# Performance work log

Measured on AMD Instinct MI355X. Metric: run time of the kernel, lower is better.

Reference implementation:

```python
import jax, jax.numpy as jnp
import numpy as np

B, L, D, H = 2, 2048, 2048, 16
HD = D // H  # 128

def setup_inputs() -> dict:
    key = jax.random.key(0)
    ks = jax.random.split(key, 12)
    s = 1.0 / np.sqrt(D)
    inp = {
        'x': jax.random.normal(ks[0], (B, L, D), jnp.float32),
        'sin': jax.random.normal(ks[1], (L, HD // 2), jnp.float32),
        'cos': jax.random.normal(ks[2], (L, HD // 2), jnp.float32),
        'mask': jnp.tril(jnp.ones((L, L), jnp.int32))[None, None],  # causal [1,1,L,L]
        'Wq': jax.random.normal(ks[3], (D, D), jnp.float32) * s,
        'bq': jnp.zeros((D,), jnp.float32),
        'Wk': jax.random.normal(ks[4], (D, D), jnp.float32) * s,
        'bk': jnp.zeros((D,), jnp.float32),
        'Wv': jax.random.normal(ks[5], (D, D), jnp.float32) * s,
        'bv': jnp.zeros((D,), jnp.float32),
        'Wo': jax.random.normal(ks[6], (D, D), jnp.float32) * s,
        'bo': jnp.zeros((D,), jnp.float32),
    }
    return inp

def reference(x, sin, cos, mask, Wq, bq, Wk, bk, Wv, bv, Wo, bo):
    Bx, Lx, Dx = x.shape
    q = (x @ Wq.T + bq).reshape(Bx, Lx, H, HD)
    k = (x @ Wk.T + bk).reshape(Bx, Lx, H, HD)
    v = (x @ Wv.T + bv).reshape(Bx, Lx, H, HD)
    half = HD // 2
    # partial rotary: note original computes q_rot*(cos - sin) (faithful)
    rot = (cos - sin)[:, None, :]  # [L,1,half]
    q = jnp.concatenate([q[..., :half] * rot, q[..., half:]], axis=-1)
    k = jnp.concatenate([k[..., :half] * rot, k[..., half:]], axis=-1)
    q = q.transpose(0, 2, 1, 3)  # [B,H,L,hd]
    k = k.transpose(0, 2, 1, 3)
    v = v.transpose(0, 2, 1, 3)
    scores = jnp.einsum('bhqd,bhkd->bhqk', q, k) / np.sqrt(HD).astype(np.float32)
    scores = jnp.where(mask == 0, -jnp.inf, scores)
    attn = jax.nn.softmax(scores, axis=-1)
    out = jnp.einsum('bhqk,bhkd->bhqd', attn, v)
    out = out.transpose(0, 2, 1, 3).reshape(Bx, Lx, Dx)
    return out @ Wo.T + bo
```

## Files before the change

kernel.cpp:

```cpp
#include <hip/hip_runtime.h>
#include <hip/hip_bf16.h>

typedef __attribute__((ext_vector_type(8))) short short8;
typedef __attribute__((ext_vector_type(4))) ushort ushort4v;
typedef __attribute__((ext_vector_type(4))) float f32x4;

#define MFMA16(A, B, C) __builtin_amdgcn_mfma_f32_16x16x32_bf16(A, B, C, 0, 0, 0)

#define GLOAD16(gp, lp)                                        \
  __builtin_amdgcn_global_load_lds(                            \
      (__attribute__((address_space(1))) void*)(gp),           \
      (__attribute__((address_space(3))) void*)(lp), 16, 0, 0)

static constexpr int Lx = 2048, Dx = 2048, Hx = 16, HDx = 128, NBx = 2;

__device__ __forceinline__ ushort f2bu(float f) {
  __hip_bfloat16 h = __float2bfloat16(f);
  union { __hip_bfloat16 h; ushort u; } v;
  v.h = h;
  return v.u;
}

__device__ __forceinline__ short8 pack8(const float4& a, const float4& b) {
  short8 r;
  r[0] = (short)f2bu(a.x); r[1] = (short)f2bu(a.y);
  r[2] = (short)f2bu(a.z); r[3] = (short)f2bu(a.w);
  r[4] = (short)f2bu(b.x); r[5] = (short)f2bu(b.y);
  r[6] = (short)f2bu(b.z); r[7] = (short)f2bu(b.w);
  return r;
}

__global__ void convert_kernel(const float* __restrict__ x,
                               const float* __restrict__ Wq,
                               const float* __restrict__ Wk,
                               const float* __restrict__ Wv,
                               const float* __restrict__ Wo,
                               ushort* __restrict__ xb, ushort* __restrict__ wqb,
                               ushort* __restrict__ wkb, ushort* __restrict__ wvb,
                               ushort* __restrict__ wob) {
  const int y = blockIdx.y;
  const float* s;
  ushort* d;
  int n;
  switch (y) {
    case 0: s = x;  d = xb;  n = NBx * Lx * Dx; break;
    case 1: s = Wq; d = wqb; n = Dx * Dx; break;
    case 2: s = Wk; d = wkb; n = Dx * Dx; break;
    case 3: s = Wv; d = wvb; n = Dx * Dx; break;
    default: s = Wo; d = wob; n = Dx * Dx; break;
  }
  const int stride = gridDim.x * blockDim.x * 8;
  for (int i = (blockIdx.x * blockDim.x + threadIdx.x) * 8; i < n; i += stride) {
    float4 a = *(const float4*)(s + i);
    float4 b = *(const float4*)(s + i + 4);
    *(short8*)(d + i) = pack8(a, b);
  }
}

__global__ __launch_bounds__(256, 2) void qkv_kernel(
    const ushort* __restrict__ xb,
    const ushort* __restrict__ wqb, const float* __restrict__ bq,
    const ushort* __restrict__ wkb, const float* __restrict__ bk,
    const ushort* __restrict__ wvb, const float* __restrict__ bv,
    const float* __restrict__ sinT, const float* __restrict__ cosT,
    ushort* __restrict__ qw, ushort* __restrict__ kw, ushort* __restrict__ vw) {
  const int z = blockIdx.z;
  const ushort* W   = (z == 0) ? wqb : (z == 1) ? wkb : wvb;
  const float* bias = (z == 0) ? bq : (z == 1) ? bk : bv;
  ushort* outp      = (z == 0) ? qw : (z == 1) ? kw : vw;

  const int bm = blockIdx.x, bn = blockIdx.y;
  const int tid = threadIdx.x;
  const int lane = tid & 63;
  const int w = tid >> 6;
  const int l15 = tid & 15, hi = (tid >> 4) & 3;
  const int wm = (w >> 1) * 64, wn = (w & 1) * 64;

  __shared__ ushort As[2][128 * 32];
  __shared__ ushort Bs[2][128 * 32];

  const int cA = w * 2;
  const int srow = cA * 16 + (lane >> 2);
  const int scol = (lane & 3) * 8;
  const ushort* aSrc = xb + (size_t)(bm * 128 + srow) * Dx + scol;
  const ushort* bSrc = W + (size_t)(bn * 128 + srow) * Dx + scol;
  const int ldsOff = cA * 512;

#define STAGE_QKV(buf, kt)                                           \
  do {                                                               \
    const ushort* ap = aSrc + (kt) * 32;                             \
    const ushort* bp = bSrc + (kt) * 32;                             \
    GLOAD16(ap, &As[buf][ldsOff]);                                   \
    GLOAD16(ap + 16 * Dx, &As[buf][ldsOff + 512]);                   \
    GLOAD16(bp, &Bs[buf][ldsOff]);                                   \
    GLOAD16(bp + 16 * Dx, &Bs[buf][ldsOff + 512]);                   \
  } while (0)

  f32x4 acc[4][4];
#pragma unroll
  for (int i = 0; i < 4; ++i)
#pragma unroll
    for (int j = 0; j < 4; ++j) acc[i][j] = {0.f, 0.f, 0.f, 0.f};

  STAGE_QKV(0, 0);
  __syncthreads();

  int cur = 0;
  for (int kt = 0; kt < 64; ++kt) {
    if (kt < 63) STAGE_QKV(cur ^ 1, kt + 1);
    short8 af[4], bf[4];
#pragma unroll
    for (int i = 0; i < 4; ++i)
      af[i] = *(const short8*)&As[cur][(wm + i * 16 + l15) * 32 + hi * 8];
#pragma unroll
    for (int j = 0; j < 4; ++j)
      bf[j] = *(const short8*)&Bs[cur][(wn + j * 16 + l15) * 32 + hi * 8];
#pragma unroll
    for (int i = 0; i < 4; ++i)
#pragma unroll
      for (int j = 0; j < 4; ++j) acc[i][j] = MFMA16(af[i], bf[j], acc[i][j]);
    __syncthreads();
    cur ^= 1;
  }
#undef STAGE_QKV

  const float rsHD = 0.08838834764831845f;
#pragma unroll
  for (int j = 0; j < 4; ++j) {
    const int n = bn * 128 + wn + j * 16 + l15;
    const int h = n >> 7, d = n & 127;
    const float bb = bias[n];
#pragma unroll
    for (int i = 0; i < 4; ++i) {
#pragma unroll
      for (int r = 0; r < 4; ++r) {
        const int m = bm * 128 + wm + i * 16 + hi * 4 + r;
        const int b = m >> 11, l = m & (Lx - 1);
        float v = acc[i][j][r] + bb;
        if (z < 2 && d < 64) v *= (cosT[l * 64 + d] - sinT[l * 64 + d]);
        if (z == 0) v *= rsHD;
        outp[(size_t)((b * Hx + h) * Lx + l) * HDx + d] = f2bu(v);
      }
    }
  }
}

__global__ __launch_bounds__(256, 2) void attn_kernel(
    const ushort* __restrict__ qw, const ushort* __restrict__ kw,
    const ushort* __restrict__ vw, ushort* __restrict__ ctx) {
  const int pair = blockIdx.x;
  const int bh = blockIdx.y;
  const int b = bh >> 4, h = bh & 15;
  const int tid = threadIdx.x;
  const int w = tid >> 6, l15 = tid & 15, hi = (tid >> 4) & 3;

  const ushort* Q = qw + (size_t)bh * Lx * HDx;
  const ushort* K = kw + (size_t)bh * Lx * HDx;
  const ushort* V = vw + (size_t)bh * Lx * HDx;

  __shared__ ushort Ks[64][136];
  __shared__ ushort Vt[128][76];
  __shared__ ushort Ps[4][16][76];

  const int skrow = tid >> 2, skd = (tid & 3) * 32;
  const int svk = (tid & 15) * 4, svd = (tid >> 4) * 8;

  for (int seg = 0; seg < 2; ++seg) {
    const int qt = seg ? (31 - pair) : pair;

    short8 qf[4];
    {
      const ushort* qr = Q + (size_t)(qt * 64 + w * 16 + l15) * HDx + hi * 8;
#pragma unroll
      for (int ds = 0; ds < 4; ++ds) qf[ds] = *(const short8*)(qr + ds * 32);
    }

    f32x4 o[8];
#pragma unroll
    for (int df = 0; df < 8; ++df) o[df] = {0.f, 0.f, 0.f, 0.f};
    float mr[4], lr[4];
#pragma unroll
    for (int r = 0; r < 4; ++r) { mr[r] = -1e30f; lr[r] = 0.f; }

    short8 kreg[4], vreg[4];
    {
      const ushort* kp = K + (size_t)skrow * HDx + skd;
      kreg[0] = *(const short8*)(kp + 0);  kreg[1] = *(const short8*)(kp + 8);
      kreg[2] = *(const short8*)(kp + 16); kreg[3] = *(const short8*)(kp + 24);
      const ushort* vp = V + (size_t)svk * HDx + svd;
      vreg[0] = *(const short8*)(vp);
      vreg[1] = *(const short8*)(vp + HDx);
      vreg[2] = *(const short8*)(vp + 2 * HDx);
      vreg[3] = *(const short8*)(vp + 3 * HDx);
    }

    for (int kv = 0; kv <= qt; ++kv) {
      __syncthreads();
      *(short8*)&Ks[skrow][skd + 0] = kreg[0];
      *(short8*)&Ks[skrow][skd + 8] = kreg[1];
      *(short8*)&Ks[skrow][skd + 16] = kreg[2];
      *(short8*)&Ks[skrow][skd + 24] = kreg[3];
#pragma unroll
      for (int j = 0; j < 8; ++j) {
        ushort4v pk;
        pk[0] = (ushort)vreg[0][j]; pk[1] = (ushort)vreg[1][j];
        pk[2] = (ushort)vreg[2][j]; pk[3] = (ushort)vreg[3][j];
        *(ushort4v*)&Vt[svd + j][svk] = pk;
      }
      __syncthreads();

      if (kv < qt) {
        const ushort* kp = K + (size_t)((kv + 1) * 64 + skrow) * HDx + skd;
        kreg[0] = *(const short8*)(kp + 0);  kreg[1] = *(const short8*)(kp + 8);
        kreg[2] = *(const short8*)(kp + 16); kreg[3] = *(const short8*)(kp + 24);
        const ushort* vp = V + (size_t)((kv + 1) * 64 + svk) * HDx + svd;
        vreg[0] = *(const short8*)(vp);
        vreg[1] = *(const short8*)(vp + HDx);
        vreg[2] = *(const short8*)(vp + 2 * HDx);
        vreg[3] = *(const short8*)(vp + 3 * HDx);
      }

      f32x4 s[4];
#pragma unroll
      for (int kf = 0; kf < 4; ++kf) s[kf] = {0.f, 0.f, 0.f, 0.f};
      __builtin_amdgcn_s_setprio(1);
#pragma unroll
      for (int kf = 0; kf < 4; ++kf)
#pragma unroll
        for (int ds = 0; ds < 4; ++ds) {
          short8 kb = *(const short8*)&Ks[kf * 16 + l15][ds * 32 + hi * 8];
          s[kf] = MFMA16(qf[ds], kb, s[kf]);
        }
      __builtin_amdgcn_s_setprio(0);

      if (kv == qt) {
#pragma unroll
        for (int kf = 0; kf < 4; ++kf)
#pragma unroll
          for (int r = 0; r < 4; ++r)
            if (kf * 16 + l15 > w * 16 + hi * 4 + r) s[kf][r] = -1e30f;
      }

      float ml[4];
#pragma unroll
      for (int r = 0; r < 4; ++r)
        ml[r] = fmaxf(fmaxf(s[0][r], s[1][r]), fmaxf(s[2][r], s[3][r]));
#pragma unroll
      for (int off = 1; off <= 8; off <<= 1)
#pragma unroll
        for (int r = 0; r < 4; ++r) ml[r] = fmaxf(ml[r], __shfl_xor(ml[r], off));
      float scl[4];
#pragma unroll
      for (int r = 0; r < 4; ++r) {
        float mn = fmaxf(mr[r], ml[r]);
        scl[r] = __expf(mr[r] - mn);
        mr[r] = mn;
      }
      float ll[4] = {0.f, 0.f, 0.f, 0.f};
#pragma unroll
      for (int kf = 0; kf < 4; ++kf)
#pragma unroll
        for (int r = 0; r < 4; ++r) {
          float p = __expf(s[kf][r] - mr[r]);
          s[kf][r] = p;
          ll[r] += p;
        }
#pragma unroll
      for (int off = 1; off <= 8; off <<= 1)
#pragma unroll
        for (int r = 0; r < 4; ++r) ll[r] += __shfl_xor(ll[r], off);
#pragma unroll
      for (int r = 0; r < 4; ++r) lr[r] = lr[r] * scl[r] + ll[r];
#pragma unroll
      for (int df = 0; df < 8; ++df)
#pragma unroll
        for (int r = 0; r < 4; ++r) o[df][r] *= scl[r];

#pragma unroll
      for (int kf = 0; kf < 4; ++kf)
#pragma unroll
        for (int r = 0; r < 4; ++r)
          Ps[w][hi * 4 + r][kf * 16 + l15] = f2bu(s[kf][r]);

      short8 pa0 = *(const short8*)&Ps[w][l15][hi * 8];
      short8 pa1 = *(const short8*)&Ps[w][l15][32 + hi * 8];
      __builtin_amdgcn_s_setprio(1);
#pragma unroll
      for (int df = 0; df < 8; ++df) {
        short8 v0 = *(const short8*)&Vt[df * 16 + l15][hi * 8];
        short8 v1 = *(const short8*)&Vt[df * 16 + l15][32 + hi * 8];
        o[df] = MFMA16(pa0, v0, o[df]);
        o[df] = MFMA16(pa1, v1, o[df]);
      }
      __builtin_amdgcn_s_setprio(0);
    }

    float inv[4];
#pragma unroll
    for (int r = 0; r < 4; ++r) inv[r] = 1.0f / lr[r];
    ushort* cp = ctx + (size_t)(b * Lx + qt * 64 + w * 16) * Dx + h * HDx;
#pragma unroll
    for (int df = 0; df < 8; ++df)
#pragma unroll
      for (int r = 0; r < 4; ++r)
        cp[(size_t)(hi * 4 + r) * Dx + df * 16 + l15] = f2bu(o[df][r] * inv[r]);
  }
}

__global__ __launch_bounds__(256, 2) void oproj_kernel(
    const ushort* __restrict__ ctx, const ushort* __restrict__ wob,
    const float* __restrict__ bo, float* __restrict__ out) {
  const int bm = blockIdx.x, bn = blockIdx.y;
  const int tid = threadIdx.x;
  const int lane = tid & 63;
  const int w = tid >> 6;
  const int l15 = tid & 15, hi = (tid >> 4) & 3;
  const int wm = (w >> 1) * 64, wn = (w & 1) * 64;

  __shared__ ushort As[2][128 * 32];
  __shared__ ushort Bs[2][128 * 32];

  const int cA = w * 2;
  const int srow = cA * 16 + (lane >> 2);
  const int scol = (lane & 3) * 8;
  const ushort* aSrc = ctx + (size_t)(bm * 128 + srow) * Dx + scol;
  const ushort* bSrc = wob + (size_t)(bn * 128 + srow) * Dx + scol;
  const int ldsOff = cA * 512;

#define STAGE_O(buf, kt)                                             \
  do {                                                               \
    const ushort* ap = aSrc + (kt) * 32;                             \
    const ushort* bp = bSrc + (kt) * 32;                             \
    GLOAD16(ap, &As[buf][ldsOff]);                                   \
    GLOAD16(ap + 16 * Dx, &As[buf][ldsOff + 512]);                   \
    GLOAD16(bp, &Bs[buf][ldsOff]);                                   \
    GLOAD16(bp + 16 * Dx, &Bs[buf][ldsOff + 512]);                   \
  } while (0)

  f32x4 acc[4][4];
#pragma unroll
  for (int i = 0; i < 4; ++i)
#pragma unroll
    for (int j = 0; j < 4; ++j) acc[i][j] = {0.f, 0.f, 0.f, 0.f};

  STAGE_O(0, 0);
  __syncthreads();

  int cur = 0;
  for (int kt = 0; kt < 64; ++kt) {
    if (kt < 63) STAGE_O(cur ^ 1, kt + 1);
    short8 af[4], bf[4];
#pragma unroll
    for (int i = 0; i < 4; ++i)
      af[i] = *(const short8*)&As[cur][(wm + i * 16 + l15) * 32 + hi * 8];
#pragma unroll
    for (int j = 0; j < 4; ++j)
      bf[j] = *(const short8*)&Bs[cur][(wn + j * 16 + l15) * 32 + hi * 8];
#pragma unroll
    for (int i = 0; i < 4; ++i)
#pragma unroll
      for (int j = 0; j < 4; ++j) acc[i][j] = MFMA16(af[i], bf[j], acc[i][j]);
    __syncthreads();
    cur ^= 1;
  }
#undef STAGE_O

#pragma unroll
  for (int j = 0; j < 4; ++j) {
    const int n = bn * 128 + wn + j * 16 + l15;
    const float bb = bo[n];
#pragma unroll
    for (int i = 0; i < 4; ++i)
#pragma unroll
      for (int r = 0; r < 4; ++r) {
        const int m = bm * 128 + wm + i * 16 + hi * 4 + r;
        out[(size_t)m * Dx + n] = acc[i][j][r] + bb;
      }
  }
}

extern "C" void kernel_launch(void* const* d_in, const int* in_sizes, int n_in,
                              void* d_out, int out_size, void* d_ws, size_t ws_size,
                              hipStream_t stream) {
  (void)in_sizes; (void)n_in; (void)out_size; (void)ws_size;
  const float* x    = (const float*)d_in[0];
  const float* sinT = (const float*)d_in[1];
  const float* cosT = (const float*)d_in[2];
  const float* Wq = (const float*)d_in[4];
  const float* bq = (const float*)d_in[5];
  const float* Wk = (const float*)d_in[6];
  const float* bk = (const float*)d_in[7];
  const float* Wv = (const float*)d_in[8];
  const float* bv = (const float*)d_in[9];
  const float* Wo = (const float*)d_in[10];
  const float* bo = (const float*)d_in[11];
  float* out = (float*)d_out;

  const size_t N = (size_t)NBx * Lx * Dx;
  const size_t M = (size_t)Dx * Dx;
  ushort* qw  = (ushort*)d_ws;
  ushort* kw  = qw + N;
  ushort* vw  = kw + N;
  ushort* ctx = vw + N;
  ushort* xb  = ctx;
  ushort* wqb = ctx + N;
  ushort* wkb = wqb + M;
  ushort* wvb = wkb + M;
  ushort* wob = wvb + M;

  convert_kernel<<<dim3(1024, 5), 256, 0, stream>>>(
      x, Wq, Wk, Wv, Wo, xb, wqb, wkb, wvb, wob);
  qkv_kernel<<<dim3(32, 16, 3), 256, 0, stream>>>(
      xb, wqb, bq, wkb, bk, wvb, bv, sinT, cosT, qw, kw, vw);
  attn_kernel<<<dim3(16, 32), 256, 0, stream>>>(qw, kw, vw, ctx);
  oproj_kernel<<<dim3(32, 16), 256, 0, stream>>>(ctx, wob, bo, out);
}
```

Before: 456.1 us.

## Use shared 256x256 tiled GEMM core with deeper pipelining for QKV and O projections

Replaces the 128x128 double-buffered GEMMs with a shared 256x256-tile, 512-thread core. It uses a 64-wide K step split into two halves, staged global-to-LDS loads issued two tiles ahead, raw s_barrier/waitcnt control, and setprio around the MFMA bursts. QKV treats the contiguous Wq/Wk/Wv buffers as one 6144-row weight matrix. The aim is higher arithmetic intensity and fewer barriers per FLOP. The trade-off is far fewer blocks (384 and 128), which may underfill the 256 CUs, plus more registers and LDS per block.

```diff
diff --git a/kernel.cpp b/kernel.cpp
--- a/kernel.cpp
+++ b/kernel.cpp
@@ -11,6 +11,10 @@
   __builtin_amdgcn_global_load_lds(                            \
       (__attribute__((address_space(1))) void*)(gp),           \
       (__attribute__((address_space(3))) void*)(lp), 16, 0, 0)
+
+#define SBAR()   asm volatile("s_barrier" ::: "memory")
+#define LGKM0()  asm volatile("s_waitcnt lgkmcnt(0)" ::: "memory")
+#define VMCNT6() asm volatile("s_waitcnt vmcnt(6)" ::: "memory")
 
 static constexpr int Lx = 2048, Dx = 2048, Hx = 16, HDx = 128, NBx = 2;
 
@@ -57,89 +61,177 @@
   }
 }
 
-__global__ __launch_bounds__(256, 2) void qkv_kernel(
-    const ushort* __restrict__ xb,
-    const ushort* __restrict__ wqb, const float* __restrict__ bq,
-    const ushort* __restrict__ wkb, const float* __restrict__ bk,
-    const ushort* __restrict__ wvb, const float* __restrict__ bv,
+__device__ __forceinline__ void gemm256_core(const ushort* __restrict__ A0,
+                                             const ushort* __restrict__ B0,
+                                             f32x4 (&acc)[8][4], const int tid) {
+  __shared__ ushort LA[2][2][8192];
+  __shared__ ushort LB[2][2][8192];
+
+  const int lane = tid & 63;
+  const int l15 = lane & 15, hi = (lane >> 4) & 3;
+  const int w = tid >> 6, wr = w >> 2, wc = w & 3;
+  constexpr int NT = 2048 / 64;
+
+  const ushort* aRow = A0 + (size_t)(tid >> 2) * Dx + (tid & 3) * 8;
+  const ushort* bRow = B0 + (size_t)(tid >> 2) * Dx + (tid & 3) * 8;
+  const int ldsT = (tid >> 2) * 32 + (tid & 3) * 8;
+
+#define STG_A(s, kk, t)                                                     \
+  do {                                                                      \
+    GLOAD16(aRow + (t) * 64 + (kk) * 32, &LA[s][kk][ldsT]);                 \
+    GLOAD16(aRow + (size_t)128 * Dx + (t) * 64 + (kk) * 32,                 \
+            &LA[s][kk][4096 + ldsT]);                                       \
+  } while (0)
+#define STG_B(s, kk, t)                                                     \
+  do {                                                                      \
+    GLOAD16(bRow + (t) * 64 + (kk) * 32, &LB[s][kk][ldsT]);                 \
+    GLOAD16(bRow + (size_t)128 * Dx + (t) * 64 + (kk) * 32,                 \
+            &LB[s][kk][4096 + ldsT]);                                       \
+  } while (0)
+
+#pragma unroll
+  for (int m = 0; m < 8; ++m)
+#pragma unroll
+    for (int n = 0; n < 4; ++n) acc[m][n] = {0.f, 0.f, 0.f, 0.f};
+
+  STG_B(0, 0, 0); STG_A(0, 0, 0); STG_B(0, 1, 0); STG_A(0, 1, 0);
+  STG_B(1, 0, 1); STG_A(1, 0, 1); STG_B(1, 1, 1);
+  VMCNT6();
+  SBAR();
+
+  const int ar0 = wr * 128 + l15;
+  const int br0 = wc * 64 + l15;
+
+  for (int t = 0; t < NT; ++t) {
+    const int s = t & 1;
+    short8 af[4], bf[4], ag[4];
+
+#pragma unroll
+    for (int m = 0; m < 4; ++m)
+      af[m] = *(const short8*)&LA[s][0][(ar0 + m * 16) * 32 + hi * 8];
+#pragma unroll
+    for (int n = 0; n < 4; ++n)
+      bf[n] = *(const short8*)&LB[s][0][(br0 + n * 16) * 32 + hi * 8];
+    if (t + 1 < NT) STG_A(s ^ 1, 1, t + 1);
+    SBAR(); LGKM0();
+    __builtin_amdgcn_s_setprio(1);
+#pragma unroll
+    for (int m = 0; m < 4; ++m)
+#pragma unroll
+      for (int n = 0; n < 4; ++n) acc[m][n] = MFMA16(af[m], bf[n], acc[m][n]);
+    __builtin_amdgcn_s_setprio(0);
+    SBAR();
+
+#pragma unroll
+    for (int m = 0; m < 4; ++m)
+      ag[m] = *(const short8*)&LA[s][0][(ar0 + (m + 4) * 16) * 32 + hi * 8];
+    if (t + 2 < NT) STG_B(s, 0, t + 2);
+    SBAR(); LGKM0();
+    __builtin_amdgcn_s_setprio(1);
+#pragma unroll
+    for (int m = 0; m < 4; ++m)
+#pragma unroll
+      for (int n = 0; n < 4; ++n)
+        acc[m + 4][n] = MFMA16(ag[m], bf[n], acc[m + 4][n]);
+    __builtin_amdgcn_s_setprio(0);
+    SBAR();
+
+#pragma unroll
+    for (int m = 0; m < 4; ++m)
+      af[m] = *(const short8*)&LA[s][1][(ar0 + m * 16) * 32 + hi * 8];
+#pragma unroll
+    for (int n = 0; n < 4; ++n)
+      bf[n] = *(const short8*)&LB[s][1][(br0 + n * 16) * 32 + hi * 8];
+    if (t + 2 < NT) STG_A(s, 0, t + 2);
+    SBAR(); LGKM0();
+    __builtin_amdgcn_s_setprio(1);
+#pragma unroll
+    for (int m = 0; m < 4; ++m)
+#pragma unroll
+      for (int n = 0; n < 4; ++n) acc[m][n] = MFMA16(af[m], bf[n], acc[m][n]);
+    __builtin_amdgcn_s_setprio(0);
+    SBAR();
+
+#pragma unroll
+    for (int m = 0; m < 4; ++m)
+      ag[m] = *(const short8*)&LA[s][1][(ar0 + (m + 4) * 16) * 32 + hi * 8];
+    if (t + 2 < NT) STG_B(s, 1, t + 2);
+    SBAR(); LGKM0();
+    __builtin_amdgcn_s_setprio(1);
+#pragma unroll
+    for (int m = 0; m < 4; ++m)
+#pragma unroll
+      for (int n = 0; n < 4; ++n)
+        acc[m + 4][n] = MFMA16(ag[m], bf[n], acc[m + 4][n]);
+    __builtin_amdgcn_s_setprio(0);
+    VMCNT6();
+    SBAR();
+  }
+#undef STG_A
+#undef STG_B
+}
+
+__global__ __launch_bounds__(512, 2) void qkv_kernel(
+    const ushort* __restrict__ xb, const ushort* __restrict__ Wall,
+    const float* __restrict__ bq, const float* __restrict__ bk,
+    const float* __restrict__ bv,
     const float* __restrict__ sinT, const float* __restrict__ cosT,
     ushort* __restrict__ qw, ushort* __restrict__ kw, ushort* __restrict__ vw) {
-  const int z = blockIdx.z;
-  const ushort* W   = (z == 0) ? wqb : (z == 1) ? wkb : wvb;
+  const int bm = blockIdx.x;
+  const int bnp = blockIdx.y;
+  const int z = bnp >> 3, bn = bnp & 7;
+  const int tid = threadIdx.x;
+
+  f32x4 acc[8][4];
+  gemm256_core(xb + (size_t)bm * 256 * Dx, Wall + (size_t)bnp * 256 * Dx, acc, tid);
+
   const float* bias = (z == 0) ? bq : (z == 1) ? bk : bv;
   ushort* outp      = (z == 0) ? qw : (z == 1) ? kw : vw;
-
-  const int bm = blockIdx.x, bn = blockIdx.y;
-  const int tid = threadIdx.x;
-  const int lane = tid & 63;
-  const int w = tid >> 6;
-  const int l15 = tid & 15, hi = (tid >> 4) & 3;
-  const int wm = (w >> 1) * 64, wn = (w & 1) * 64;
-
-  __shared__ ushort As[2][128 * 32];
-  __shared__ ushort Bs[2][128 * 32];
-
-  const int cA = w * 2;
-  const int srow = cA * 16 + (lane >> 2);
-  const int scol = (lane & 3) * 8;
-  const ushort* aSrc = xb + (size_t)(bm * 128 + srow) * Dx + scol;
-  const ushort* bSrc = W + (size_t)(bn * 128 + srow) * Dx + scol;
-  const int ldsOff = cA * 512;
-
-#define STAGE_QKV(buf, kt)                                           \
-  do {                                                               \
-    const ushort* ap = aSrc + (kt) * 32;                             \
-    const ushort* bp = bSrc + (kt) * 32;                             \
-    GLOAD16(ap, &As[buf][ldsOff]);                                   \
-    GLOAD16(ap + 16 * Dx, &As[buf][ldsOff + 512]);                   \
-    GLOAD16(bp, &Bs[buf][ldsOff]);                                   \
-    GLOAD16(bp + 16 * Dx, &Bs[buf][ldsOff + 512]);                   \
-  } while (0)
-
-  f32x4 acc[4][4];
-#pragma unroll
-  for (int i = 0; i < 4; ++i)
-#pragma unroll
-    for (int j = 0; j < 4; ++j) acc[i][j] = {0.f, 0.f, 0.f, 0.f};
-
-  STAGE_QKV(0, 0);
-  __syncthreads();
-
-  int cur = 0;
-  for (int kt = 0; kt < 64; ++kt) {
-    if (kt < 63) STAGE_QKV(cur ^ 1, kt + 1);
-    short8 af[4], bf[4];
-#pragma unroll
-    for (int i = 0; i < 4; ++i)
-      af[i] = *(const short8*)&As[cur][(wm + i * 16 + l15) * 32 + hi * 8];
-#pragma unroll
-    for (int j = 0; j < 4; ++j)
-      bf[j] = *(const short8*)&Bs[cur][(wn + j * 16 + l15) * 32 + hi * 8];
-#pragma unroll
-    for (int i = 0; i < 4; ++i)
-#pragma unroll
-      for (int j = 0; j < 4; ++j) acc[i][j] = MFMA16(af[i], bf[j], acc[i][j]);
-    __syncthreads();
-    cur ^= 1;
-  }
-#undef STAGE_QKV
-
+  const int lane = tid & 63, l15 = lane & 15, hi = (lane >> 4) & 3;
+  const int w = tid >> 6, wr = w >> 2, wc = w & 3;
   const float rsHD = 0.08838834764831845f;
 #pragma unroll
-  for (int j = 0; j < 4; ++j) {
-    const int n = bn * 128 + wn + j * 16 + l15;
-    const int h = n >> 7, d = n & 127;
-    const float bb = bias[n];
-#pragma unroll
-    for (int i = 0; i < 4; ++i) {
+  for (int n = 0; n < 4; ++n) {
+    const int nc = bn * 256 + wc * 64 + n * 16 + l15;
+    const int h = nc >> 7, d = nc & 127;
+    const float bb = bias[nc];
+#pragma unroll
+    for (int m = 0; m < 8; ++m) {
 #pragma unroll
       for (int r = 0; r < 4; ++r) {
-        const int m = bm * 128 + wm + i * 16 + hi * 4 + r;
-        const int b = m >> 11, l = m & (Lx - 1);
-        float v = acc[i][j][r] + bb;
+        const int mg = bm * 256 + wr * 128 + m * 16 + hi * 4 + r;
+        const int b = mg >> 11, l = mg & (Lx - 1);
+        float v = acc[m][n][r] + bb;
         if (z < 2 && d < 64) v *= (cosT[l * 64 + d] - sinT[l * 64 + d]);
         if (z == 0) v *= rsHD;
         outp[(size_t)((b * Hx + h) * Lx + l) * HDx + d] = f2bu(v);
+      }
+    }
+  }
+}
+
+__global__ __launch_bounds__(512, 2) void oproj_kernel(
+    const ushort* __restrict__ ctx, const ushort* __restrict__ wob,
+    const float* __restrict__ bo, float* __restrict__ out) {
+  const int bm = blockIdx.x;
+  const int bn = blockIdx.y;
+  const int tid = threadIdx.x;
+
+  f32x4 acc[8][4];
+  gemm256_core(ctx + (size_t)bm * 256 * Dx, wob + (size_t)bn * 256 * Dx, acc, tid);
+
+  const int lane = tid & 63, l15 = lane & 15, hi = (lane >> 4) & 3;
+  const int w = tid >> 6, wr = w >> 2, wc = w & 3;
+#pragma unroll
+  for (int n = 0; n < 4; ++n) {
+    const int nc = bn * 256 + wc * 64 + n * 16 + l15;
+    const float bb = bo[nc];
+#pragma unroll
+    for (int m = 0; m < 8; ++m) {
+#pragma unroll
+      for (int r = 0; r < 4; ++r) {
+        const int mg = bm * 256 + wr * 128 + m * 16 + hi * 4 + r;
+        out[(size_t)mg * Dx + nc] = acc[m][n][r] + bb;
       }
     }
   }
@@ -304,78 +396,6 @@
 #pragma unroll
       for (int r = 0; r < 4; ++r)
         cp[(size_t)(hi * 4 + r) * Dx + df * 16 + l15] = f2bu(o[df][r] * inv[r]);
-  }
-}
-
-__global__ __launch_bounds__(256, 2) void oproj_kernel(
-    const ushort* __restrict__ ctx, const ushort* __restrict__ wob,
-    const float* __restrict__ bo, float* __restrict__ out) {
-  const int bm = blockIdx.x, bn = blockIdx.y;
-  const int tid = threadIdx.x;
-  const int lane = tid & 63;
-  const int w = tid >> 6;
-  const int l15 = tid & 15, hi = (tid >> 4) & 3;
-  const int wm = (w >> 1) * 64, wn = (w & 1) * 64;
-
-  __shared__ ushort As[2][128 * 32];
-  __shared__ ushort Bs[2][128 * 32];
-
-  const int cA = w * 2;
-  const int srow = cA * 16 + (lane >> 2);
-  const int scol = (lane & 3) * 8;
-  const ushort* aSrc = ctx + (size_t)(bm * 128 + srow) * Dx + scol;
-  const ushort* bSrc = wob + (size_t)(bn * 128 + srow) * Dx + scol;
-  const int ldsOff = cA * 512;
-
-#define STAGE_O(buf, kt)                                             \
-  do {                                                               \
-    const ushort* ap = aSrc + (kt) * 32;                             \
-    const ushort* bp = bSrc + (kt) * 32;                             \
-    GLOAD16(ap, &As[buf][ldsOff]);                                   \
-    GLOAD16(ap + 16 * Dx, &As[buf][ldsOff + 512]);                   \
-    GLOAD16(bp, &Bs[buf][ldsOff]);                                   \
-    GLOAD16(bp + 16 * Dx, &Bs[buf][ldsOff + 512]);                   \
-  } while (0)
-
-  f32x4 acc[4][4];
-#pragma unroll
-  for (int i = 0; i < 4; ++i)
-#pragma unroll
-    for (int j = 0; j < 4; ++j) acc[i][j] = {0.f, 0.f, 0.f, 0.f};
-
-  STAGE_O(0, 0);
-  __syncthreads();
-
-  int cur = 0;
-  for (int kt = 0; kt < 64; ++kt) {
-    if (kt < 63) STAGE_O(cur ^ 1, kt + 1);
-    short8 af[4], bf[4];
-#pragma unroll
-    for (int i = 0; i < 4; ++i)
-      af[i] = *(const short8*)&As[cur][(wm + i * 16 + l15) * 32 + hi * 8];
-#pragma unroll
-    for (int j = 0; j < 4; ++j)
-      bf[j] = *(const short8*)&Bs[cur][(wn + j * 16 + l15) * 32 + hi * 8];
-#pragma unroll
-    for (int i = 0; i < 4; ++i)
-#pragma unroll
-      for (int j = 0; j < 4; ++j) acc[i][j] = MFMA16(af[i], bf[j], acc[i][j]);
-    __syncthreads();
-    cur ^= 1;
-  }
-#undef STAGE_O
-
-#pragma unroll
-  for (int j = 0; j < 4; ++j) {
-    const int n = bn * 128 + wn + j * 16 + l15;
-    const float bb = bo[n];
-#pragma unroll
-    for (int i = 0; i < 4; ++i)
-#pragma unroll
-      for (int r = 0; r < 4; ++r) {
-        const int m = bm * 128 + wm + i * 16 + hi * 4 + r;
-        out[(size_t)m * Dx + n] = acc[i][j][r] + bb;
-      }
   }
 }
 
@@ -407,11 +427,12 @@
   ushort* wkb = wqb + M;
   ushort* wvb = wkb + M;
   ushort* wob = wvb + M;
+  (void)wkb; (void)wvb;
 
   convert_kernel<<<dim3(1024, 5), 256, 0, stream>>>(
       x, Wq, Wk, Wv, Wo, xb, wqb, wkb, wvb, wob);
-  qkv_kernel<<<dim3(32, 16, 3), 256, 0, stream>>>(
-      xb, wqb, bq, wkb, bk, wvb, bv, sinT, cosT, qw, kw, vw);
+  qkv_kernel<<<dim3(16, 24), 512, 0, stream>>>(
+      xb, wqb, bq, bk, bv, sinT, cosT, qw, kw, vw);
   attn_kernel<<<dim3(16, 32), 256, 0, stream>>>(qw, kw, vw, ctx);
-  oproj_kernel<<<dim3(32, 16), 256, 0, stream>>>(ctx, wob, bo, out);
-}
+  oproj_kernel<<<dim3(16, 8), 512, 0, stream>>>(ctx, wob, bo, out);
+}
```

New measurement: 527.3 us. +15.6%, slower.

## Widen attention blocks to 128 query rows with eight waves sharing KV tiles

Applied to the files above, without the earlier changes.

The attention kernel now runs 512-thread blocks of eight waves, each block covering 128 query rows instead of 64. Every 64-row K/V tile staged in shared memory is therefore reused by twice as many waves, halving global K/V traffic and the per-block staging work. The cooperative K/V load is re-split across 512 threads, and the causal mask is adjusted for the two diagonal tiles. In exchange, the grid shrinks to 256 blocks, and the lower-half waves compute one fully masked tile per segment.

```diff
diff --git a/kernel.cpp b/kernel.cpp
--- a/kernel.cpp
+++ b/kernel.cpp
@@ -145,7 +145,7 @@
   }
 }
 
-__global__ __launch_bounds__(256, 2) void attn_kernel(
+__global__ __launch_bounds__(512, 2) void attn_kernel(
     const ushort* __restrict__ qw, const ushort* __restrict__ kw,
     const ushort* __restrict__ vw, ushort* __restrict__ ctx) {
   const int pair = blockIdx.x;
@@ -160,17 +160,18 @@
 
   __shared__ ushort Ks[64][136];
   __shared__ ushort Vt[128][76];
-  __shared__ ushort Ps[4][16][76];
-
-  const int skrow = tid >> 2, skd = (tid & 3) * 32;
-  const int svk = (tid & 15) * 4, svd = (tid >> 4) * 8;
+  __shared__ ushort Ps[8][16][76];
+
+  const int skrow = tid >> 3, skc = (tid & 7) * 16;
+  const int svk = (tid & 15) * 4, svd = (tid >> 4) * 4;
 
   for (int seg = 0; seg < 2; ++seg) {
-    const int qt = seg ? (31 - pair) : pair;
+    const int qt = seg ? (15 - pair) : pair;
+    const int nkv = 2 * qt + 2;
 
     short8 qf[4];
     {
-      const ushort* qr = Q + (size_t)(qt * 64 + w * 16 + l15) * HDx + hi * 8;
+      const ushort* qr = Q + (size_t)(qt * 128 + w * 16 + l15) * HDx + hi * 8;
 #pragma unroll
       for (int ds = 0; ds < 4; ++ds) qf[ds] = *(const short8*)(qr + ds * 32);
     }
@@ -182,42 +183,37 @@
 #pragma unroll
     for (int r = 0; r < 4; ++r) { mr[r] = -1e30f; lr[r] = 0.f; }
 
-    short8 kreg[4], vreg[4];
+    short8 kreg0, kreg1;
+    ushort4v vreg[4];
     {
-      const ushort* kp = K + (size_t)skrow * HDx + skd;
-      kreg[0] = *(const short8*)(kp + 0);  kreg[1] = *(const short8*)(kp + 8);
-      kreg[2] = *(const short8*)(kp + 16); kreg[3] = *(const short8*)(kp + 24);
+      const ushort* kp = K + (size_t)skrow * HDx + skc;
+      kreg0 = *(const short8*)(kp);
+      kreg1 = *(const short8*)(kp + 8);
       const ushort* vp = V + (size_t)svk * HDx + svd;
-      vreg[0] = *(const short8*)(vp);
-      vreg[1] = *(const short8*)(vp + HDx);
-      vreg[2] = *(const short8*)(vp + 2 * HDx);
-      vreg[3] = *(const short8*)(vp + 3 * HDx);
+#pragma unroll
+      for (int j = 0; j < 4; ++j) vreg[j] = *(const ushort4v*)(vp + j * HDx);
     }
 
-    for (int kv = 0; kv <= qt; ++kv) {
+    for (int kv = 0; kv < nkv; ++kv) {
       __syncthreads();
-      *(short8*)&Ks[skrow][skd + 0] = kreg[0];
-      *(short8*)&Ks[skrow][skd + 8] = kreg[1];
-      *(short8*)&Ks[skrow][skd + 16] = kreg[2];
-      *(short8*)&Ks[skrow][skd + 24] = kreg[3];
-#pragma unroll
-      for (int j = 0; j < 8; ++j) {
+      *(short8*)&Ks[skrow][skc] = kreg0;
+      *(short8*)&Ks[skrow][skc + 8] = kreg1;
+#pragma unroll
+      for (int i = 0; i < 4; ++i) {
         ushort4v pk;
-        pk[0] = (ushort)vreg[0][j]; pk[1] = (ushort)vreg[1][j];
-        pk[2] = (ushort)vreg[2][j]; pk[3] = (ushort)vreg[3][j];
-        *(ushort4v*)&Vt[svd + j][svk] = pk;
+        pk[0] = vreg[0][i]; pk[1] = vreg[1][i];
+        pk[2] = vreg[2][i]; pk[3] = vreg[3][i];
+        *(ushort4v*)&Vt[svd + i][svk] = pk;
       }
       __syncthreads();
 
-      if (kv < qt) {
-        const ushort* kp = K + (size_t)((kv + 1) * 64 + skrow) * HDx + skd;
-        kreg[0] = *(const short8*)(kp + 0);  kreg[1] = *(const short8*)(kp + 8);
-        kreg[2] = *(const short8*)(kp + 16); kreg[3] = *(const short8*)(kp + 24);
+      if (kv + 1 < nkv) {
+        const ushort* kp = K + (size_t)((kv + 1) * 64 + skrow) * HDx + skc;
+        kreg0 = *(const short8*)(kp);
+        kreg1 = *(const short8*)(kp + 8);
         const ushort* vp = V + (size_t)((kv + 1) * 64 + svk) * HDx + svd;
-        vreg[0] = *(const short8*)(vp);
-        vreg[1] = *(const short8*)(vp + HDx);
-        vreg[2] = *(const short8*)(vp + 2 * HDx);
-        vreg[3] = *(const short8*)(vp + 3 * HDx);
+#pragma unroll
+        for (int j = 0; j < 4; ++j) vreg[j] = *(const ushort4v*)(vp + j * HDx);
       }
 
       f32x4 s[4];
@@ -233,12 +229,13 @@
         }
       __builtin_amdgcn_s_setprio(0);
 
-      if (kv == qt) {
+      if (kv >= 2 * qt) {
+        const int coff = (kv - 2 * qt) * 64;
 #pragma unroll
         for (int kf = 0; kf < 4; ++kf)
 #pragma unroll
           for (int r = 0; r < 4; ++r)
-            if (kf * 16 + l15 > w * 16 + hi * 4 + r) s[kf][r] = -1e30f;
+            if (coff + kf * 16 + l15 > w * 16 + hi * 4 + r) s[kf][r] = -1e30f;
       }
 
       float ml[4];
@@ -298,7 +295,7 @@
     float inv[4];
 #pragma unroll
     for (int r = 0; r < 4; ++r) inv[r] = 1.0f / lr[r];
-    ushort* cp = ctx + (size_t)(b * Lx + qt * 64 + w * 16) * Dx + h * HDx;
+    ushort* cp = ctx + (size_t)(b * Lx + qt * 128 + w * 16) * Dx + h * HDx;
 #pragma unroll
     for (int df = 0; df < 8; ++df)
 #pragma unroll
@@ -412,6 +409,6 @@
       x, Wq, Wk, Wv, Wo, xb, wqb, wkb, wvb, wob);
   qkv_kernel<<<dim3(32, 16, 3), 256, 0, stream>>>(
       xb, wqb, bq, wkb, bk, wvb, bv, sinT, cosT, qw, kw, vw);
-  attn_kernel<<<dim3(16, 32), 256, 0, stream>>>(qw, kw, vw, ctx);
+  attn_kernel<<<dim3(8, 32), 512, 0, stream>>>(qw, kw, vw, ctx);
   oproj_kernel<<<dim3(32, 16), 256, 0, stream>>>(ctx, wob, bo, out);
 }
```

Measured after the change: 454.9 us. No clear change (-0.3%).
